# Performance work log

Hardware: AMD Instinct MI355X
Metric: run time of the kernel (lower is better)

## Reference

```python
import jax, jax.numpy as jnp
import numpy as np

B, N, DIM, H, DH = 4, 2048, 512, 8, 64  # patches_num == N (required by the math)
INNER = H * DH
SCALE = DH ** -0.5


def setup_inputs() -> dict:
    key = jax.random.key(0)
    ks = jax.random.split(key, 6)
    s = lambda fan_in: 1.0 / np.sqrt(fan_in)
    return {
        "x": jax.random.normal(ks[0], (B, N, DIM), dtype=jnp.float32),
        "w_qkfv": jax.random.normal(ks[1], (DIM, 4 * INNER), dtype=jnp.float32) * s(DIM),
        "w_scales": jax.random.normal(ks[2], (DH, N), dtype=jnp.float32) * s(DH),
        "b_scales": jax.random.normal(ks[3], (N,), dtype=jnp.float32) * s(DH),
        "w_out": jax.random.normal(ks[4], (INNER, DIM), dtype=jnp.float32) * s(INNER),
        "b_out": jax.random.normal(ks[5], (DIM,), dtype=jnp.float32) * s(INNER),
    }


def reference(x, w_qkfv, w_scales, b_scales, w_out, b_out):
    # Fused qkfv projection: [B,N,4*INNER]
    qkfv = x @ w_qkfv
    q, k, f, v = jnp.split(qkfv, 4, axis=-1)
    split_heads = lambda t: t.reshape(B, N, H, DH).transpose(0, 2, 1, 3)  # b h n d
    q, k, f, v = map(split_heads, (q, k, f, v))

    # q @ k^T * scale -> [b,h,n,n]
    scores = jnp.einsum("bhid,bhjd->bhij", q, k) * SCALE
    attn = jax.nn.softmax(scores, axis=-1)

    # f^T @ v -> [b,h,d,d], then Linear(dim_head -> patches_num) -> [b,h,d,n]
    poss_value = jnp.einsum("bhnd,bhne->bhde", f, v)
    poss_value = poss_value @ w_scales + b_scales  # [b,h,d,n]

    # attn @ poss_value^T -> [b,h,n,d]
    out = jnp.einsum("bhij,bhdj->bhid", attn, poss_value)
    out = out.transpose(0, 2, 1, 3).reshape(B, N, INNER)  # b n (h d)

    # to_out (dropout=0 / eval mode -> identity)
    return out @ w_out + b_out
```

## Files before the change

kernel.cpp:

```cpp
#include <hip/hip_runtime.h>
#include <stdint.h>

#define N_SEQ 2048
#define QKFV_COLS 2048

typedef __attribute__((ext_vector_type(8))) __bf16 bf16x8;
typedef __attribute__((ext_vector_type(4))) __bf16 bf16x4;
typedef __attribute__((ext_vector_type(4))) float f32x4;
typedef __attribute__((ext_vector_type(16))) float f32x16;

#if __has_builtin(__builtin_amdgcn_exp2f)
#define EXP2(x) __builtin_amdgcn_exp2f(x)
#else
#define EXP2(x) exp2f(x)
#endif

__device__ __forceinline__ f32x4 mfma16(bf16x8 a, bf16x8 b, f32x4 c) {
  return __builtin_amdgcn_mfma_f32_16x16x32_bf16(a, b, c, 0, 0, 0);
}
__device__ __forceinline__ f32x16 mfma32(bf16x8 a, bf16x8 b, f32x16 c) {
  return __builtin_amdgcn_mfma_f32_32x32x16_bf16(a, b, c, 0, 0, 0);
}

__device__ __forceinline__ void glds16(const void* g, void* l) {
  __builtin_amdgcn_global_load_lds(
      (__attribute__((address_space(1))) uint32_t*)(uintptr_t)g,
      (__attribute__((address_space(3))) uint32_t*)l, 16, 0, 0);
}

__global__ __launch_bounds__(256) void prep_kernel(const float* __restrict__ x,
                                                   __bf16* __restrict__ xbf,
                                                   const float* __restrict__ wqk,
                                                   __bf16* __restrict__ wqT,
                                                   const float* __restrict__ wo,
                                                   __bf16* __restrict__ woT,
                                                   const float* __restrict__ wsc,
                                                   __bf16* __restrict__ wscT) {
  const int t = threadIdx.x;
  int bid = blockIdx.x;
  if (bid < 2048) {
    size_t i = (size_t)bid * 2048 + t * 8;
    const float* p = x + i;
    bf16x8 o;
#pragma unroll
    for (int j = 0; j < 8; ++j) o[j] = (__bf16)p[j];
    *(bf16x8*)(xbf + i) = o;
    return;
  }
  bid -= 2048;
  const float* in;
  __bf16* outp;
  int R, C, rt, ct;
  if (bid < 256) { in = wqk; outp = wqT; R = 512; C = 2048; rt = bid >> 5; ct = bid & 31; }
  else if (bid < 320) { int b2 = bid - 256; in = wo; outp = woT; R = 512; C = 512; rt = b2 >> 3; ct = b2 & 7; }
  else { int b2 = bid - 320; in = wsc; outp = wscT; R = 64; C = 2048; rt = 0; ct = b2; }
  __shared__ __bf16 tile[64][72];
  const int r0 = rt * 64, c0 = ct * 64;
  {
    const int r = t >> 2, cq = (t & 3) * 16;
    const float* src = in + (size_t)(r0 + r) * C + c0 + cq;
#pragma unroll
    for (int q = 0; q < 4; ++q) {
      f32x4 v = *(const f32x4*)(src + q * 4);
#pragma unroll
      for (int e = 0; e < 4; ++e) tile[r][cq + q * 4 + e] = (__bf16)v[e];
    }
  }
  __syncthreads();
  {
    const int c = t >> 2, rq = (t & 3) * 16;
    __bf16* dst = outp + (size_t)(c0 + c) * R + r0 + rq;
    bf16x8 o0, o1;
#pragma unroll
    for (int j = 0; j < 8; ++j) { o0[j] = tile[rq + j][c]; o1[j] = tile[rq + 8 + j][c]; }
    *(bf16x8*)dst = o0;
    *(bf16x8*)(dst + 8) = o1;
  }
}

__global__ __launch_bounds__(512, 4) void gemm_qkfv_kernel(const __bf16* __restrict__ A,
                                                           const __bf16* __restrict__ Bt,
                                                           __bf16* __restrict__ C,
                                                           __bf16* __restrict__ fT,
                                                           __bf16* __restrict__ vT) {
  __shared__ alignas(16) __bf16 Ab[2][128 * 32];
  __shared__ alignas(16) __bf16 Bb[2][256 * 32];
  const int K = 512, N = 2048;
  const int t = threadIdx.x;
  const int w = t >> 6;
  const int lane = t & 63;
  const int l15 = lane & 15;
  const int q4 = lane >> 4;
  const int g4 = q4 * 4;
  const int wr = w >> 2, wc = w & 3;
  const int bid = blockIdx.x;
  const int n0 = (bid & 7) * 256;
  const int m0 = (bid >> 3) * 128;

  const __bf16* srcA;
  const __bf16* srcB[2];
  {
    int s = t, r = s >> 2, u = (s & 3) ^ (r & 3);
    srcA = A + (size_t)(m0 + r) * K + u * 8;
  }
#pragma unroll
  for (int c = 0; c < 2; ++c) {
    int s = c * 512 + t, r = s >> 2, u = (s & 3) ^ (r & 3);
    srcB[c] = Bt + (size_t)(n0 + r) * K + u * 8;
  }

  f32x4 acc[4][4];
#pragma unroll
  for (int m = 0; m < 4; ++m)
#pragma unroll
    for (int n = 0; n < 4; ++n) acc[m][n] = (f32x4){0.f, 0.f, 0.f, 0.f};

  glds16(srcA, &Ab[0][t * 8]);
  glds16(srcB[0], &Bb[0][t * 8]);
  glds16(srcB[1], &Bb[0][(512 + t) * 8]);

  for (int kt = 0; kt < 16; ++kt) {
    const int cur = kt & 1;
    asm volatile("s_waitcnt vmcnt(0)" ::: "memory");
    __builtin_amdgcn_s_barrier();
    if (kt < 15) {
      const int k0 = (kt + 1) * 32;
      glds16(srcA + k0, &Ab[cur ^ 1][t * 8]);
      glds16(srcB[0] + k0, &Bb[cur ^ 1][t * 8]);
      glds16(srcB[1] + k0, &Bb[cur ^ 1][(512 + t) * 8]);
    }
    bf16x8 af[4], bf[4];
#pragma unroll
    for (int m = 0; m < 4; ++m) {
      const int R = wr * 64 + m * 16 + l15;
      af[m] = *(const bf16x8*)&Ab[cur][R * 32 + ((q4 ^ (R & 3)) * 8)];
    }
#pragma unroll
    for (int n = 0; n < 4; ++n) {
      const int R = wc * 64 + n * 16 + l15;
      bf[n] = *(const bf16x8*)&Bb[cur][R * 32 + ((q4 ^ (R & 3)) * 8)];
    }
    __builtin_amdgcn_s_setprio(1);
#pragma unroll
    for (int m = 0; m < 4; ++m)
#pragma unroll
      for (int n = 0; n < 4; ++n) acc[m][n] = mfma16(af[m], bf[n], acc[m][n]);
    __builtin_amdgcn_s_setprio(0);
    __builtin_amdgcn_s_barrier();
  }

  if (n0 < 1024) {
#pragma unroll
    for (int m = 0; m < 4; ++m)
#pragma unroll
      for (int n = 0; n < 4; ++n) {
        const int col = n0 + wc * 64 + n * 16 + l15;
        const int row = m0 + wr * 64 + m * 16 + g4;
#pragma unroll
        for (int r = 0; r < 4; ++r)
          C[(size_t)(row + r) * N + col] = (__bf16)acc[m][n][r];
      }
  } else {
    __bf16* T = (n0 < 1536) ? fT : vT;
    const int cbase = (n0 < 1536) ? 1024 : 1536;
#pragma unroll
    for (int m = 0; m < 4; ++m)
#pragma unroll
      for (int n = 0; n < 4; ++n) {
        const int hc = n0 + wc * 64 + n * 16 + l15 - cbase;
        const int h = hc >> 6, d = hc & 63;
        const int row = m0 + wr * 64 + m * 16 + g4;
        const int b = row >> 11, nl = row & 2047;
        bf16x4 pk;
#pragma unroll
        for (int r = 0; r < 4; ++r) pk[r] = (__bf16)acc[m][n][r];
        *(bf16x4*)&T[(size_t)((b * 8 + h) * 64 + d) * 2048 + nl] = pk;
      }
  }
}

__global__ __launch_bounds__(512, 4) void gemm_out_kernel(const __bf16* __restrict__ A,
                                                          const __bf16* __restrict__ Bt,
                                                          float* __restrict__ out,
                                                          const float* __restrict__ bias) {
  __shared__ alignas(16) __bf16 As[128 * 32];
  __shared__ alignas(16) __bf16 Bs[64 * 32];
  const int K = 512, N = 512;
  const int t = threadIdx.x;
  const int w = t >> 6;
  const int lane = t & 63;
  const int l15 = lane & 15;
  const int q4 = lane >> 4;
  const int g4 = q4 * 4;
  const int wr = w >> 1, wc = w & 1;
  const int m0 = blockIdx.x * 128, n0 = blockIdx.y * 64;

  const __bf16* srcA;
  const __bf16* srcB;
  {
    int s = t, r = s >> 2, u = (s & 3) ^ (r & 3);
    srcA = A + (size_t)(m0 + r) * K + u * 8;
    srcB = Bt + (size_t)(n0 + (r & 63)) * K + u * 8;
  }

  f32x4 acc[2][2];
#pragma unroll
  for (int m = 0; m < 2; ++m)
#pragma unroll
    for (int n = 0; n < 2; ++n) acc[m][n] = (f32x4){0.f, 0.f, 0.f, 0.f};

  for (int kt = 0; kt < 16; ++kt) {
    const int k0 = kt * 32;
    glds16(srcA + k0, &As[t * 8]);
    if (t < 256) glds16(srcB + k0, &Bs[t * 8]);
    __syncthreads();
    bf16x8 af[2], bf[2];
#pragma unroll
    for (int m = 0; m < 2; ++m) {
      const int R = wr * 32 + m * 16 + l15;
      af[m] = *(const bf16x8*)&As[R * 32 + ((q4 ^ (R & 3)) * 8)];
    }
#pragma unroll
    for (int n = 0; n < 2; ++n) {
      const int R = wc * 32 + n * 16 + l15;
      bf[n] = *(const bf16x8*)&Bs[R * 32 + ((q4 ^ (R & 3)) * 8)];
    }
#pragma unroll
    for (int m = 0; m < 2; ++m)
#pragma unroll
      for (int n = 0; n < 2; ++n) acc[m][n] = mfma16(af[m], bf[n], acc[m][n]);
    __syncthreads();
  }

#pragma unroll
  for (int m = 0; m < 2; ++m)
#pragma unroll
    for (int n = 0; n < 2; ++n) {
      const int col = n0 + wc * 32 + n * 16 + l15;
      const float bv = bias[col];
      const int row = m0 + wr * 32 + m * 16 + g4;
#pragma unroll
      for (int r = 0; r < 4; ++r)
        out[(size_t)(row + r) * N + col] = acc[m][n][r] + bv;
    }
}

__global__ __launch_bounds__(256) void fvmm_kernel(const __bf16* __restrict__ fT,
                                                   const __bf16* __restrict__ vT,
                                                   float* __restrict__ fvp) {
  __shared__ alignas(16) __bf16 As[2 * 8192];
  __shared__ alignas(16) __bf16 Bs[2 * 8192];
  const int t = threadIdx.x;
  const int w = t >> 6;
  const int lane = t & 63;
  const int l15 = lane & 15;
  const int q4 = lane >> 4;
  const int g4 = q4 * 4;
  const int sl = blockIdx.x;
  const int bh = blockIdx.y;
  const int k0 = sl * 256;
  const __bf16* A = fT + (size_t)bh * 131072 + k0;
  const __bf16* B = vT + (size_t)bh * 131072 + k0;

#pragma unroll
  for (int kt = 0; kt < 2; ++kt)
#pragma unroll
    for (int c = 0; c < 4; ++c) {
      int slot = c * 256 + t;
      int r = slot >> 4, u = (slot & 15) ^ (r & 7);
      glds16(A + (size_t)r * 2048 + kt * 128 + u * 8, &As[kt * 8192 + (c * 256 + w * 64) * 8]);
      glds16(B + (size_t)r * 2048 + kt * 128 + u * 8, &Bs[kt * 8192 + (c * 256 + w * 64) * 8]);
    }
  asm volatile("s_waitcnt vmcnt(0)" ::: "memory");
  __syncthreads();

  f32x4 acc[4];
#pragma unroll
  for (int nb = 0; nb < 4; ++nb) acc[nb] = (f32x4){0.f, 0.f, 0.f, 0.f};
  const int arow = w * 16 + l15;
#pragma unroll
  for (int ks = 0; ks < 8; ++ks) {
    const int kt = ks >> 2;
    const int ku = (ks & 3) * 4 + q4;
    bf16x8 a = *(const bf16x8*)&As[kt * 8192 + arow * 128 + ((ku ^ (arow & 7)) * 8)];
#pragma unroll
    for (int nb = 0; nb < 4; ++nb) {
      const int br = nb * 16 + l15;
      bf16x8 bb = *(const bf16x8*)&Bs[kt * 8192 + br * 128 + ((ku ^ (br & 7)) * 8)];
      acc[nb] = mfma16(a, bb, acc[nb]);
    }
  }
  float* dst = fvp + (size_t)(sl * 32 + bh) * 4096;
#pragma unroll
  for (int nb = 0; nb < 4; ++nb)
#pragma unroll
    for (int r = 0; r < 4; ++r)
      dst[(w * 16 + g4 + r) * 64 + nb * 16 + l15] = acc[nb][r];
}

__global__ __launch_bounds__(256) void pvmat2_kernel(const float* __restrict__ fvp,
                                                     const __bf16* __restrict__ wscT,
                                                     const float* __restrict__ bsc,
                                                     __bf16* __restrict__ pvm) {
  __shared__ alignas(16) __bf16 fs[64 * 72];
  __shared__ alignas(16) __bf16 Ws[128 * 64];
  const int t = threadIdx.x;
  const int w = t >> 6;
  const int lane = t & 63;
  const int l15 = lane & 15;
  const int q4 = lane >> 4;
  const int g4 = q4 * 4;
  const int bh = blockIdx.y;
  const int j0 = blockIdx.x * 128;

#pragma unroll
  for (int c = 0; c < 4; ++c) {
    int slot = c * 256 + t;
    int r = slot >> 3, u = (slot & 7) ^ (r & 7);
    glds16(wscT + (size_t)(j0 + r) * 64 + u * 8, &Ws[(c * 256 + w * 64) * 8]);
  }
#pragma unroll
  for (int qq = 0; qq < 4; ++qq) {
    int idx = t * 16 + qq * 4;
    f32x4 s = (f32x4){0.f, 0.f, 0.f, 0.f};
#pragma unroll
    for (int sl = 0; sl < 8; ++sl)
      s += *(const f32x4*)&fvp[(size_t)(sl * 32 + bh) * 4096 + idx];
    bf16x4 pk;
#pragma unroll
    for (int e = 0; e < 4; ++e) pk[e] = (__bf16)s[e];
    *(bf16x4*)&fs[(idx >> 6) * 72 + (idx & 63)] = pk;
  }
  asm volatile("s_waitcnt vmcnt(0)" ::: "memory");
  __syncthreads();

  f32x4 acc[8];
#pragma unroll
  for (int nb = 0; nb < 8; ++nb) {
    float bv = bsc[j0 + nb * 16 + l15];
    acc[nb] = (f32x4){bv, bv, bv, bv};
  }
  const int arow = w * 16 + l15;
#pragma unroll
  for (int ks = 0; ks < 2; ++ks) {
    bf16x8 a = *(const bf16x8*)&fs[arow * 72 + ks * 32 + q4 * 8];
#pragma unroll
    for (int nb = 0; nb < 8; ++nb) {
      const int jr = nb * 16 + l15;
      bf16x8 bb = *(const bf16x8*)&Ws[jr * 64 + (((ks * 4 + q4) ^ (jr & 7)) * 8)];
      acc[nb] = mfma16(a, bb, acc[nb]);
    }
  }
  __bf16* dst = pvm + (size_t)bh * 131072 + (size_t)j0;
#pragma unroll
  for (int nb = 0; nb < 8; ++nb)
#pragma unroll
    for (int r = 0; r < 4; ++r)
      dst[(size_t)(w * 16 + g4 + r) * 2048 + nb * 16 + l15] = (__bf16)acc[nb][r];
}

__global__ __launch_bounds__(512, 4) void attn_kernel(const __bf16* __restrict__ qkfv,
                                                      const __bf16* __restrict__ pvm,
                                                      __bf16* __restrict__ obuf) {
  __shared__ alignas(16) char smem[65536];
  __bf16* Kb = (__bf16*)smem;
  __bf16* Vb = (__bf16*)(smem + 32768);
  const int t = threadIdx.x;
  const int w = t >> 6;
  const int g = w >> 2;
  const int wq = w & 3;
  const int lane = t & 63;
  const int ln = lane & 31;
  const int hi = lane >> 5;
  const int p = blockIdx.x;
  const int bh = (p & 7) * 4 + ((p >> 3) & 3);
  const int iblk = p >> 5;
  const int b = bh >> 3, h = bh & 7;
  const int irow = iblk * 128 + wq * 32 + ln;
  const float K1 = 0.18033688f;
  const int swz = ln & 7;

  bf16x8 q[4];
  const __bf16* qrow = qkfv + (size_t)(b * N_SEQ + irow) * QKFV_COLS + h * 64 + hi * 8;
#pragma unroll
  for (int kf = 0; kf < 4; ++kf) {
    bf16x8 raw = *(const bf16x8*)(qrow + kf * 16);
#pragma unroll
    for (int e = 0; e < 8; ++e) q[kf][e] = (__bf16)((float)raw[e] * K1);
  }

  const int tg = t & 255;
  const __bf16* ksrc[2];
  const __bf16* vsrc[2];
#pragma unroll
  for (int it = 0; it < 2; ++it) {
    int s = it * 256 + tg;
    int r = s >> 3;
    int u = (s & 7) ^ (r & 7);
    ksrc[it] = qkfv + (size_t)(b * N_SEQ + g * 1024 + r) * QKFV_COLS + 512 + h * 64 + u * 8;
    vsrc[it] = pvm + ((size_t)bh * 64 + r) * 2048 + g * 1024 + u * 8;
  }

  auto stage = [&](int buf, int jt) {
#pragma unroll
    for (int it = 0; it < 2; ++it) {
      glds16(ksrc[it] + ((size_t)jt << 17), &Kb[(g * 2 + buf) * 4096 + (it * 256 + wq * 64) * 8]);
      glds16(vsrc[it] + jt * 64, &Vb[(g * 2 + buf) * 4096 + (it * 256 + wq * 64) * 8]);
    }
  };

  f32x16 o0, o1;
#pragma unroll
  for (int e = 0; e < 16; ++e) { o0[e] = 0.f; o1[e] = 0.f; }
  float lrl = 0.f;

  stage(0, 0);

  for (int jt = 0; jt < 16; ++jt) {
    asm volatile("s_waitcnt vmcnt(0)" ::: "memory");
    __builtin_amdgcn_s_barrier();
    if (jt < 15) stage((jt & 1) ^ 1, jt + 1);
    const int kc = (g * 2 + (jt & 1)) * 4096;

    f32x16 s0, s1;
#pragma unroll
    for (int e = 0; e < 16; ++e) { s0[e] = 0.f; s1[e] = 0.f; }
    __builtin_amdgcn_s_setprio(1);
#pragma unroll
    for (int kf = 0; kf < 4; ++kf) {
      bf16x8 k0 = *(const bf16x8*)&Kb[kc + (ln) * 64 + (((2 * kf + hi) ^ swz) * 8)];
      bf16x8 k1 = *(const bf16x8*)&Kb[kc + (32 + ln) * 64 + (((2 * kf + hi) ^ swz) * 8)];
      s0 = mfma32(k0, q[kf], s0);
      s1 = mfma32(k1, q[kf], s1);
    }
    __builtin_amdgcn_s_setprio(0);

#pragma unroll
    for (int e = 0; e < 16; ++e) s0[e] = EXP2(s0[e]);
#pragma unroll
    for (int e = 0; e < 16; ++e) s1[e] = EXP2(s1[e]);
    float a8[8];
#pragma unroll
    for (int e = 0; e < 8; ++e)
      a8[e] = (s0[e] + s0[e + 8]) + (s1[e] + s1[e + 8]);
    lrl += ((a8[0] + a8[4]) + (a8[1] + a8[5])) + ((a8[2] + a8[6]) + (a8[3] + a8[7]));

    bf16x8 pa[4];
#pragma unroll
    for (int kk = 0; kk < 4; ++kk) {
      const f32x16& sf = (kk < 2) ? s0 : s1;
      const int rb = (kk & 1) * 8;
      uint32_t a0, a1, b0, b1;
      asm("v_cvt_pk_bf16_f32 %0, %1, %2" : "=v"(a0) : "v"(sf[rb + 0]), "v"(sf[rb + 1]));
      asm("v_cvt_pk_bf16_f32 %0, %1, %2" : "=v"(a1) : "v"(sf[rb + 2]), "v"(sf[rb + 3]));
      asm("v_cvt_pk_bf16_f32 %0, %1, %2" : "=v"(b0) : "v"(sf[rb + 4]), "v"(sf[rb + 5]));
      asm("v_cvt_pk_bf16_f32 %0, %1, %2" : "=v"(b1) : "v"(sf[rb + 6]), "v"(sf[rb + 7]));
      asm("v_permlane32_swap_b32 %0, %1" : "+v"(a0), "+v"(b0));
      asm("v_permlane32_swap_b32 %0, %1" : "+v"(a1), "+v"(b1));
      union { uint32_t u[4]; bf16x8 v; } cv;
      cv.u[0] = a0; cv.u[1] = a1; cv.u[2] = b0; cv.u[3] = b1;
      pa[kk] = cv.v;
    }

    __builtin_amdgcn_s_setprio(1);
#pragma unroll
    for (int kk = 0; kk < 4; ++kk) {
      bf16x8 v0 = *(const bf16x8*)&Vb[kc + (ln) * 64 + (((2 * kk + hi) ^ swz) * 8)];
      bf16x8 v1 = *(const bf16x8*)&Vb[kc + (32 + ln) * 64 + (((2 * kk + hi) ^ swz) * 8)];
      o0 = mfma32(v0, pa[kk], o0);
      o1 = mfma32(v1, pa[kk], o1);
    }
    __builtin_amdgcn_s_setprio(0);
  }

  lrl += __shfl_xor(lrl, 32);

  __syncthreads();
  float* Om = (float*)smem;
  if (w >= 4) {
    const int base = ((w - 4) * 64 + lane) * 33;
#pragma unroll
    for (int e = 0; e < 16; ++e) { Om[base + e] = o0[e]; Om[base + 16 + e] = o1[e]; }
    Om[base + 32] = lrl;
  }
  __syncthreads();
  if (w < 4) {
    const int base = (w * 64 + lane) * 33;
#pragma unroll
    for (int e = 0; e < 16; ++e) { o0[e] += Om[base + e]; o1[e] += Om[base + 16 + e]; }
    lrl += Om[base + 32];

    const float inv = 1.0f / lrl;
    const size_t orow = (size_t)(b * N_SEQ + irow) * 512 + h * 64;
#pragma unroll
    for (int df = 0; df < 2; ++df) {
      const f32x16& oo = df ? o1 : o0;
#pragma unroll
      for (int gg = 0; gg < 4; ++gg) {
        bf16x4 pk;
#pragma unroll
        for (int e = 0; e < 4; ++e) pk[e] = (__bf16)(oo[gg * 4 + e] * inv);
        *(bf16x4*)(obuf + orow + df * 32 + gg * 8 + hi * 4) = pk;
      }
    }
  }
}

extern "C" void kernel_launch(void* const* d_in, const int* in_sizes, int n_in,
                              void* d_out, int out_size, void* d_ws, size_t ws_size,
                              hipStream_t stream) {
  (void)in_sizes; (void)n_in; (void)out_size; (void)ws_size;
  const float* x   = (const float*)d_in[0];
  const float* wqk = (const float*)d_in[1];
  const float* wsc = (const float*)d_in[2];
  const float* bsc = (const float*)d_in[3];
  const float* wo  = (const float*)d_in[4];
  const float* bo  = (const float*)d_in[5];
  float* out = (float*)d_out;

  char* p = (char*)d_ws;
  __bf16* xbf  = (__bf16*)p;  p += (size_t)8192 * 512 * 2;
  __bf16* wqT  = (__bf16*)p;  p += (size_t)2048 * 512 * 2;
  __bf16* woT  = (__bf16*)p;  p += (size_t)512 * 512 * 2;
  __bf16* wscT = (__bf16*)p;  p += (size_t)2048 * 64 * 2;
  __bf16* qkfv = (__bf16*)p;  p += (size_t)8192 * 2048 * 2;
  __bf16* pvm  = (__bf16*)p;  p += (size_t)32 * 64 * 2048 * 2;
  __bf16* obuf = (__bf16*)p;  p += (size_t)8192 * 512 * 2;
  float* fvp = (float*)xbf;
  __bf16* fT = obuf;
  __bf16* vT = pvm;

  prep_kernel<<<dim3(2400), dim3(256), 0, stream>>>(x, xbf, wqk, wqT, wo, woT, wsc, wscT);
  gemm_qkfv_kernel<<<dim3(512), dim3(512), 0, stream>>>(xbf, wqT, qkfv, fT, vT);
  fvmm_kernel<<<dim3(8, 32), dim3(256), 0, stream>>>(fT, vT, fvp);
  pvmat2_kernel<<<dim3(16, 32), dim3(256), 0, stream>>>(fvp, wscT, bsc, pvm);
  attn_kernel<<<dim3(512), dim3(512), 0, stream>>>(qkfv, pvm, obuf);
  gemm_out_kernel<<<dim3(64, 8), dim3(512), 0, stream>>>(obuf, woT, out, bo);
}
```

Before: 111.1 us.

## Halve attention block threads, each wave handling 64 query rows for K/V reuse

The attention kernel now runs 256 threads per block instead of 512. Each wave processes two 32-row query sub-blocks, so the K fragments loaded from LDS are reused across both sub-blocks and the V fragments feed four MFMAs instead of two. This cuts LDS read traffic per unit of compute. In exchange it raises register pressure, with four output accumulators and two sets of Q registers, lowers the wave count per block, and requires each thread to issue twice as many global-to-LDS staging loads.

```diff
diff --git a/kernel.cpp b/kernel.cpp
--- a/kernel.cpp
+++ b/kernel.cpp
@@ -359,7 +359,7 @@
       dst[(size_t)(w * 16 + g4 + r) * 2048 + nb * 16 + l15] = (__bf16)acc[nb][r];
 }
 
-__global__ __launch_bounds__(512, 4) void attn_kernel(const __bf16* __restrict__ qkfv,
+__global__ __launch_bounds__(256, 2) void attn_kernel(const __bf16* __restrict__ qkfv,
                                                       const __bf16* __restrict__ pvm,
                                                       __bf16* __restrict__ obuf) {
   __shared__ alignas(16) char smem[65536];
@@ -367,8 +367,8 @@
   __bf16* Vb = (__bf16*)(smem + 32768);
   const int t = threadIdx.x;
   const int w = t >> 6;
-  const int g = w >> 2;
-  const int wq = w & 3;
+  const int g = w >> 1;
+  const int wq = w & 1;
   const int lane = t & 63;
   const int ln = lane & 31;
   const int hi = lane >> 5;
@@ -376,25 +376,30 @@
   const int bh = (p & 7) * 4 + ((p >> 3) & 3);
   const int iblk = p >> 5;
   const int b = bh >> 3, h = bh & 7;
-  const int irow = iblk * 128 + wq * 32 + ln;
   const float K1 = 0.18033688f;
   const int swz = ln & 7;
 
-  bf16x8 q[4];
-  const __bf16* qrow = qkfv + (size_t)(b * N_SEQ + irow) * QKFV_COLS + h * 64 + hi * 8;
-#pragma unroll
-  for (int kf = 0; kf < 4; ++kf) {
-    bf16x8 raw = *(const bf16x8*)(qrow + kf * 16);
-#pragma unroll
-    for (int e = 0; e < 8; ++e) q[kf][e] = (__bf16)((float)raw[e] * K1);
-  }
-
-  const int tg = t & 255;
-  const __bf16* ksrc[2];
-  const __bf16* vsrc[2];
-#pragma unroll
-  for (int it = 0; it < 2; ++it) {
-    int s = it * 256 + tg;
+  bf16x8 qa[4], qb[4];
+  {
+    const __bf16* qr = qkfv + (size_t)(b * N_SEQ + iblk * 128 + wq * 64 + ln) * QKFV_COLS + h * 64 + hi * 8;
+#pragma unroll
+    for (int kf = 0; kf < 4; ++kf) {
+      bf16x8 r0 = *(const bf16x8*)(qr + kf * 16);
+      bf16x8 r1 = *(const bf16x8*)(qr + 32 * QKFV_COLS + kf * 16);
+#pragma unroll
+      for (int e = 0; e < 8; ++e) {
+        qa[kf][e] = (__bf16)((float)r0[e] * K1);
+        qb[kf][e] = (__bf16)((float)r1[e] * K1);
+      }
+    }
+  }
+
+  const int tg = t & 127;
+  const __bf16* ksrc[4];
+  const __bf16* vsrc[4];
+#pragma unroll
+  for (int it = 0; it < 4; ++it) {
+    int s = it * 128 + tg;
     int r = s >> 3;
     int u = (s & 7) ^ (r & 7);
     ksrc[it] = qkfv + (size_t)(b * N_SEQ + g * 1024 + r) * QKFV_COLS + 512 + h * 64 + u * 8;
@@ -403,16 +408,16 @@
 
   auto stage = [&](int buf, int jt) {
 #pragma unroll
-    for (int it = 0; it < 2; ++it) {
-      glds16(ksrc[it] + ((size_t)jt << 17), &Kb[(g * 2 + buf) * 4096 + (it * 256 + wq * 64) * 8]);
-      glds16(vsrc[it] + jt * 64, &Vb[(g * 2 + buf) * 4096 + (it * 256 + wq * 64) * 8]);
+    for (int it = 0; it < 4; ++it) {
+      glds16(ksrc[it] + ((size_t)jt << 17), &Kb[(g * 2 + buf) * 4096 + (it * 128 + tg) * 8]);
+      glds16(vsrc[it] + jt * 64, &Vb[(g * 2 + buf) * 4096 + (it * 128 + tg) * 8]);
     }
   };
 
-  f32x16 o0, o1;
-#pragma unroll
-  for (int e = 0; e < 16; ++e) { o0[e] = 0.f; o1[e] = 0.f; }
-  float lrl = 0.f;
+  f32x16 o00, o01, o10, o11;
+#pragma unroll
+  for (int e = 0; e < 16; ++e) { o00[e] = 0.f; o01[e] = 0.f; o10[e] = 0.f; o11[e] = 0.f; }
+  float lr0 = 0.f, lr1 = 0.f;
 
   stage(0, 0);
 
@@ -422,44 +427,54 @@
     if (jt < 15) stage((jt & 1) ^ 1, jt + 1);
     const int kc = (g * 2 + (jt & 1)) * 4096;
 
-    f32x16 s0, s1;
-#pragma unroll
-    for (int e = 0; e < 16; ++e) { s0[e] = 0.f; s1[e] = 0.f; }
-    __builtin_amdgcn_s_setprio(1);
+    bf16x8 k0f[4], k1f[4];
 #pragma unroll
     for (int kf = 0; kf < 4; ++kf) {
-      bf16x8 k0 = *(const bf16x8*)&Kb[kc + (ln) * 64 + (((2 * kf + hi) ^ swz) * 8)];
-      bf16x8 k1 = *(const bf16x8*)&Kb[kc + (32 + ln) * 64 + (((2 * kf + hi) ^ swz) * 8)];
-      s0 = mfma32(k0, q[kf], s0);
-      s1 = mfma32(k1, q[kf], s1);
-    }
-    __builtin_amdgcn_s_setprio(0);
-
-#pragma unroll
-    for (int e = 0; e < 16; ++e) s0[e] = EXP2(s0[e]);
-#pragma unroll
-    for (int e = 0; e < 16; ++e) s1[e] = EXP2(s1[e]);
-    float a8[8];
-#pragma unroll
-    for (int e = 0; e < 8; ++e)
-      a8[e] = (s0[e] + s0[e + 8]) + (s1[e] + s1[e + 8]);
-    lrl += ((a8[0] + a8[4]) + (a8[1] + a8[5])) + ((a8[2] + a8[6]) + (a8[3] + a8[7]));
-
-    bf16x8 pa[4];
-#pragma unroll
-    for (int kk = 0; kk < 4; ++kk) {
-      const f32x16& sf = (kk < 2) ? s0 : s1;
-      const int rb = (kk & 1) * 8;
-      uint32_t a0, a1, b0, b1;
-      asm("v_cvt_pk_bf16_f32 %0, %1, %2" : "=v"(a0) : "v"(sf[rb + 0]), "v"(sf[rb + 1]));
-      asm("v_cvt_pk_bf16_f32 %0, %1, %2" : "=v"(a1) : "v"(sf[rb + 2]), "v"(sf[rb + 3]));
-      asm("v_cvt_pk_bf16_f32 %0, %1, %2" : "=v"(b0) : "v"(sf[rb + 4]), "v"(sf[rb + 5]));
-      asm("v_cvt_pk_bf16_f32 %0, %1, %2" : "=v"(b1) : "v"(sf[rb + 6]), "v"(sf[rb + 7]));
-      asm("v_permlane32_swap_b32 %0, %1" : "+v"(a0), "+v"(b0));
-      asm("v_permlane32_swap_b32 %0, %1" : "+v"(a1), "+v"(b1));
-      union { uint32_t u[4]; bf16x8 v; } cv;
-      cv.u[0] = a0; cv.u[1] = a1; cv.u[2] = b0; cv.u[3] = b1;
-      pa[kk] = cv.v;
+      k0f[kf] = *(const bf16x8*)&Kb[kc + (ln) * 64 + (((2 * kf + hi) ^ swz) * 8)];
+      k1f[kf] = *(const bf16x8*)&Kb[kc + (32 + ln) * 64 + (((2 * kf + hi) ^ swz) * 8)];
+    }
+
+    bf16x8 pa0[4], pa1[4];
+#pragma unroll
+    for (int sb = 0; sb < 2; ++sb) {
+      f32x16 s0, s1;
+#pragma unroll
+      for (int e = 0; e < 16; ++e) { s0[e] = 0.f; s1[e] = 0.f; }
+      __builtin_amdgcn_s_setprio(1);
+#pragma unroll
+      for (int kf = 0; kf < 4; ++kf) {
+        bf16x8 qf = sb == 0 ? qa[kf] : qb[kf];
+        s0 = mfma32(k0f[kf], qf, s0);
+        s1 = mfma32(k1f[kf], qf, s1);
+      }
+      __builtin_amdgcn_s_setprio(0);
+
+#pragma unroll
+      for (int e = 0; e < 16; ++e) s0[e] = EXP2(s0[e]);
+#pragma unroll
+      for (int e = 0; e < 16; ++e) s1[e] = EXP2(s1[e]);
+      float a8[8];
+#pragma unroll
+      for (int e = 0; e < 8; ++e)
+        a8[e] = (s0[e] + s0[e + 8]) + (s1[e] + s1[e + 8]);
+      float ls = ((a8[0] + a8[4]) + (a8[1] + a8[5])) + ((a8[2] + a8[6]) + (a8[3] + a8[7]));
+      if (sb == 0) lr0 += ls; else lr1 += ls;
+
+#pragma unroll
+      for (int kk = 0; kk < 4; ++kk) {
+        const f32x16& sf = (kk < 2) ? s0 : s1;
+        const int rb = (kk & 1) * 8;
+        uint32_t a0, a1, b0, b1;
+        asm("v_cvt_pk_bf16_f32 %0, %1, %2" : "=v"(a0) : "v"(sf[rb + 0]), "v"(sf[rb + 1]));
+        asm("v_cvt_pk_bf16_f32 %0, %1, %2" : "=v"(a1) : "v"(sf[rb + 2]), "v"(sf[rb + 3]));
+        asm("v_cvt_pk_bf16_f32 %0, %1, %2" : "=v"(b0) : "v"(sf[rb + 4]), "v"(sf[rb + 5]));
+        asm("v_cvt_pk_bf16_f32 %0, %1, %2" : "=v"(b1) : "v"(sf[rb + 6]), "v"(sf[rb + 7]));
+        asm("v_permlane32_swap_b32 %0, %1" : "+v"(a0), "+v"(b0));
+        asm("v_permlane32_swap_b32 %0, %1" : "+v"(a1), "+v"(b1));
+        union { uint32_t u[4]; bf16x8 v; } cv;
+        cv.u[0] = a0; cv.u[1] = a1; cv.u[2] = b0; cv.u[3] = b1;
+        if (sb == 0) pa0[kk] = cv.v; else pa1[kk] = cv.v;
+      }
     }
 
     __builtin_amdgcn_s_setprio(1);
@@ -467,40 +482,60 @@
     for (int kk = 0; kk < 4; ++kk) {
       bf16x8 v0 = *(const bf16x8*)&Vb[kc + (ln) * 64 + (((2 * kk + hi) ^ swz) * 8)];
       bf16x8 v1 = *(const bf16x8*)&Vb[kc + (32 + ln) * 64 + (((2 * kk + hi) ^ swz) * 8)];
-      o0 = mfma32(v0, pa[kk], o0);
-      o1 = mfma32(v1, pa[kk], o1);
+      o00 = mfma32(v0, pa0[kk], o00);
+      o01 = mfma32(v1, pa0[kk], o01);
+      o10 = mfma32(v0, pa1[kk], o10);
+      o11 = mfma32(v1, pa1[kk], o11);
     }
     __builtin_amdgcn_s_setprio(0);
   }
 
-  lrl += __shfl_xor(lrl, 32);
+  lr0 += __shfl_xor(lr0, 32);
+  lr1 += __shfl_xor(lr1, 32);
 
   __syncthreads();
   float* Om = (float*)smem;
-  if (w >= 4) {
-    const int base = ((w - 4) * 64 + lane) * 33;
-#pragma unroll
-    for (int e = 0; e < 16; ++e) { Om[base + e] = o0[e]; Om[base + 16 + e] = o1[e]; }
-    Om[base + 32] = lrl;
+  if (w >= 2) {
+    const int base = ((w - 2) * 64 + lane) * 67;
+#pragma unroll
+    for (int e = 0; e < 16; ++e) {
+      Om[base + e] = o00[e];
+      Om[base + 16 + e] = o01[e];
+      Om[base + 32 + e] = o10[e];
+      Om[base + 48 + e] = o11[e];
+    }
+    Om[base + 64] = lr0;
+    Om[base + 65] = lr1;
   }
   __syncthreads();
-  if (w < 4) {
-    const int base = (w * 64 + lane) * 33;
-#pragma unroll
-    for (int e = 0; e < 16; ++e) { o0[e] += Om[base + e]; o1[e] += Om[base + 16 + e]; }
-    lrl += Om[base + 32];
-
-    const float inv = 1.0f / lrl;
-    const size_t orow = (size_t)(b * N_SEQ + irow) * 512 + h * 64;
-#pragma unroll
-    for (int df = 0; df < 2; ++df) {
-      const f32x16& oo = df ? o1 : o0;
-#pragma unroll
-      for (int gg = 0; gg < 4; ++gg) {
-        bf16x4 pk;
-#pragma unroll
-        for (int e = 0; e < 4; ++e) pk[e] = (__bf16)(oo[gg * 4 + e] * inv);
-        *(bf16x4*)(obuf + orow + df * 32 + gg * 8 + hi * 4) = pk;
+  if (w < 2) {
+    const int base = (w * 64 + lane) * 67;
+#pragma unroll
+    for (int e = 0; e < 16; ++e) {
+      o00[e] += Om[base + e];
+      o01[e] += Om[base + 16 + e];
+      o10[e] += Om[base + 32 + e];
+      o11[e] += Om[base + 48 + e];
+    }
+    lr0 += Om[base + 64];
+    lr1 += Om[base + 65];
+
+    const float inv0 = 1.0f / lr0;
+    const float inv1 = 1.0f / lr1;
+#pragma unroll
+    for (int sb = 0; sb < 2; ++sb) {
+      const float inv = sb == 0 ? inv0 : inv1;
+      const size_t orow = (size_t)(b * N_SEQ + iblk * 128 + wq * 64 + sb * 32 + ln) * 512 + h * 64;
+#pragma unroll
+      for (int df = 0; df < 2; ++df) {
+        const f32x16& oo = sb == 0 ? (df ? o01 : o00) : (df ? o11 : o10);
+#pragma unroll
+        for (int gg = 0; gg < 4; ++gg) {
+          bf16x4 pk;
+#pragma unroll
+          for (int e = 0; e < 4; ++e) pk[e] = (__bf16)(oo[gg * 4 + e] * inv);
+          *(bf16x4*)(obuf + orow + df * 32 + gg * 8 + hi * 4) = pk;
+        }
       }
     }
   }
@@ -534,6 +569,6 @@
   gemm_qkfv_kernel<<<dim3(512), dim3(512), 0, stream>>>(xbf, wqT, qkfv, fT, vT);
   fvmm_kernel<<<dim3(8, 32), dim3(256), 0, stream>>>(fT, vT, fvp);
   pvmat2_kernel<<<dim3(16, 32), dim3(256), 0, stream>>>(fvp, wscT, bsc, pvm);
-  attn_kernel<<<dim3(512), dim3(512), 0, stream>>>(qkfv, pvm, obuf);
+  attn_kernel<<<dim3(512), dim3(256), 0, stream>>>(qkfv, pvm, obuf);
   gemm_out_kernel<<<dim3(64, 8), dim3(512), 0, stream>>>(obuf, woT, out, bo);
 }
```

Result: slower. 115.5 us (+3.9%).

## Double-buffer LDS loads in output GEMM and remap block indices

Applied to the files above, without the earlier changes.

The output projection GEMM now double-buffers its A/B tiles in LDS, so the global-to-LDS load for the next K step is issued before the MFMAs on the current step. It also uses a 1D grid with a remapped block index and raises wave priority around the MFMA block. The aim is to hide load latency that the old load-then-sync loop exposed. It doubles the LDS footprint and keeps a barrier at the end of each iteration. The remap is effectively the same order as the old 2D grid.

```diff
diff --git a/kernel.cpp b/kernel.cpp
--- a/kernel.cpp
+++ b/kernel.cpp
@@ -183,8 +183,8 @@
                                                           const __bf16* __restrict__ Bt,
                                                           float* __restrict__ out,
                                                           const float* __restrict__ bias) {
-  __shared__ alignas(16) __bf16 As[128 * 32];
-  __shared__ alignas(16) __bf16 Bs[64 * 32];
+  __shared__ alignas(16) __bf16 Ab[2][128 * 32];
+  __shared__ alignas(16) __bf16 Bb[2][64 * 32];
   const int K = 512, N = 512;
   const int t = threadIdx.x;
   const int w = t >> 6;
@@ -193,7 +193,9 @@
   const int q4 = lane >> 4;
   const int g4 = q4 * 4;
   const int wr = w >> 1, wc = w & 1;
-  const int m0 = blockIdx.x * 128, n0 = blockIdx.y * 64;
+  const int bid = blockIdx.x;
+  const int m0 = (((bid & 7) | (((bid >> 3) & 7) << 3))) * 128;
+  const int n0 = (bid >> 6) * 64;
 
   const __bf16* srcA;
   const __bf16* srcB;
@@ -209,27 +211,36 @@
 #pragma unroll
     for (int n = 0; n < 2; ++n) acc[m][n] = (f32x4){0.f, 0.f, 0.f, 0.f};
 
+  glds16(srcA, &Ab[0][t * 8]);
+  if (t < 256) glds16(srcB, &Bb[0][t * 8]);
+
   for (int kt = 0; kt < 16; ++kt) {
-    const int k0 = kt * 32;
-    glds16(srcA + k0, &As[t * 8]);
-    if (t < 256) glds16(srcB + k0, &Bs[t * 8]);
-    __syncthreads();
+    const int cur = kt & 1;
+    asm volatile("s_waitcnt vmcnt(0)" ::: "memory");
+    __builtin_amdgcn_s_barrier();
+    if (kt < 15) {
+      const int k0 = (kt + 1) * 32;
+      glds16(srcA + k0, &Ab[cur ^ 1][t * 8]);
+      if (t < 256) glds16(srcB + k0, &Bb[cur ^ 1][t * 8]);
+    }
     bf16x8 af[2], bf[2];
 #pragma unroll
     for (int m = 0; m < 2; ++m) {
       const int R = wr * 32 + m * 16 + l15;
-      af[m] = *(const bf16x8*)&As[R * 32 + ((q4 ^ (R & 3)) * 8)];
+      af[m] = *(const bf16x8*)&Ab[cur][R * 32 + ((q4 ^ (R & 3)) * 8)];
     }
 #pragma unroll
     for (int n = 0; n < 2; ++n) {
       const int R = wc * 32 + n * 16 + l15;
-      bf[n] = *(const bf16x8*)&Bs[R * 32 + ((q4 ^ (R & 3)) * 8)];
-    }
+      bf[n] = *(const bf16x8*)&Bb[cur][R * 32 + ((q4 ^ (R & 3)) * 8)];
+    }
+    __builtin_amdgcn_s_setprio(1);
 #pragma unroll
     for (int m = 0; m < 2; ++m)
 #pragma unroll
       for (int n = 0; n < 2; ++n) acc[m][n] = mfma16(af[m], bf[n], acc[m][n]);
-    __syncthreads();
+    __builtin_amdgcn_s_setprio(0);
+    __builtin_amdgcn_s_barrier();
   }
 
 #pragma unroll
@@ -535,5 +546,5 @@
   fvmm_kernel<<<dim3(8, 32), dim3(256), 0, stream>>>(fT, vT, fvp);
   pvmat2_kernel<<<dim3(16, 32), dim3(256), 0, stream>>>(fvp, wscT, bsc, pvm);
   attn_kernel<<<dim3(512), dim3(512), 0, stream>>>(qkfv, pvm, obuf);
-  gemm_out_kernel<<<dim3(64, 8), dim3(512), 0, stream>>>(obuf, woT, out, bo);
-}
+  gemm_out_kernel<<<dim3(512), dim3(512), 0, stream>>>(obuf, woT, out, bo);
+}
```

Result: no change. 110.7 us (-0.4%).
